# Optimization experiments

Hardware: AMD Instinct MI355X
Metric: run time of the kernel (lower is better)

Reference implementation:

```python
import jax, jax.numpy as jnp
import numpy as np

B, NH, T, D = 2, 16, 2048, 64

def setup_inputs() -> dict:
    key = jax.random.key(0)
    kq, kk, kv = jax.random.split(key, 3)
    Q = jax.random.normal(kq, (B, NH, T, D), dtype=jnp.float32)
    K = jax.random.normal(kk, (B, NH, T, D), dtype=jnp.float32)
    V = jax.random.normal(kv, (B, NH, T, D), dtype=jnp.float32)
    return {"Q": Q, "K": K, "V": V}

def reference(Q, K, V):
    # scores: [B, nh, T, T]
    Dh = Q.shape[-1]
    scale = 1.0 / jnp.sqrt(jnp.asarray(Dh, Q.dtype))
    scores = jnp.einsum('bhtd,bhsd->bhts', Q, K) * scale
    Tq = Q.shape[2]
    causal = jnp.tril(jnp.ones((Tq, Tq), dtype=bool))
    scores = jnp.where(causal, scores, jnp.asarray(-jnp.inf, scores.dtype))
    attn = jax.nn.softmax(scores, axis=-1)
    return jnp.einsum('bhts,bhsd->bhtd', attn, V)
```

## Files before the change

### kernel.cpp

```cpp
#include <hip/hip_runtime.h>
#include <hip/hip_bf16.h>


typedef __bf16 bf16;
typedef __bf16 bf16x2 __attribute__((ext_vector_type(2)));
typedef __bf16 bf16x4 __attribute__((ext_vector_type(4)));
typedef __bf16 bf16x8 __attribute__((ext_vector_type(8)));
typedef float floatx4 __attribute__((ext_vector_type(4)));

#define T_SEQ 2048
#define DH 64
#define TKS 32
#define BHN 32
#define CEXP 0.18033688011112042f

__device__ __forceinline__ void gload16(const bf16* g, bf16* l) {
    __builtin_amdgcn_global_load_lds(
        (const __attribute__((address_space(1))) void*)g,
        (__attribute__((address_space(3))) void*)l, 16, 0, 0);
}

__global__ __launch_bounds__(256) void prep(const float* __restrict__ K,
                                            const float* __restrict__ V,
                                            bf16* __restrict__ Kb,
                                            bf16* __restrict__ Vt) {
    const int bid = (int)blockIdx.x;
    const int tid = (int)threadIdx.x;
    if (bid < 512) {
        size_t i = ((size_t)bid * 256 + tid) * 8;
        #pragma unroll
        for (int it = 0; it < 4; ++it) {
            float4 a = *(const float4*)(K + i + 0);
            float4 b = *(const float4*)(K + i + 4);
            bf16x8 o;
            o[0]=(bf16)(a.x*CEXP); o[1]=(bf16)(a.y*CEXP); o[2]=(bf16)(a.z*CEXP); o[3]=(bf16)(a.w*CEXP);
            o[4]=(bf16)(b.x*CEXP); o[5]=(bf16)(b.y*CEXP); o[6]=(bf16)(b.z*CEXP); o[7]=(bf16)(b.w*CEXP);
            *(bf16x8*)(Kb + i) = o;
            i += (size_t)512 * 256 * 8;
        }
        return;
    }
    __shared__ bf16 tile[2][64][72];
    const int vb = bid - 512;
    const int bh = vb & (BHN - 1);
    const int tp = (vb >> 5) * 128;
    #pragma unroll
    for (int tt = 0; tt < 2; ++tt) {
        const int r = tid >> 2;
        const int c = (tid & 3) * 16;
        const float* s = V + ((size_t)bh * T_SEQ + tp + tt * 64 + r) * DH + c;
        float4 f0 = *(const float4*)(s + 0);
        float4 f1 = *(const float4*)(s + 4);
        float4 f2 = *(const float4*)(s + 8);
        float4 f3 = *(const float4*)(s + 12);
        bf16x8 p0, p1;
        p0[0]=(bf16)f0.x; p0[1]=(bf16)f0.y; p0[2]=(bf16)f0.z; p0[3]=(bf16)f0.w;
        p0[4]=(bf16)f1.x; p0[5]=(bf16)f1.y; p0[6]=(bf16)f1.z; p0[7]=(bf16)f1.w;
        p1[0]=(bf16)f2.x; p1[1]=(bf16)f2.y; p1[2]=(bf16)f2.z; p1[3]=(bf16)f2.w;
        p1[4]=(bf16)f3.x; p1[5]=(bf16)f3.y; p1[6]=(bf16)f3.z; p1[7]=(bf16)f3.w;
        *(bf16x8*)&tile[tt][r][c + 0] = p0;
        *(bf16x8*)&tile[tt][r][c + 8] = p1;
    }
    __syncthreads();
    #pragma unroll
    for (int tt = 0; tt < 2; ++tt) {
        const int d   = tid >> 2;
        const int tch = (tid & 3) * 16;
        bf16x8 o0, o1;
        #pragma unroll
        for (int j = 0; j < 8; ++j) { o0[j] = tile[tt][tch + j][d]; o1[j] = tile[tt][tch + 8 + j][d]; }
        bf16* o = Vt + ((size_t)bh * DH + d) * T_SEQ + tp + tt * 64 + tch;
        *(bf16x8*)(o + 0) = o0;
        *(bf16x8*)(o + 8) = o1;
    }
}

__global__ __launch_bounds__(256, 2)
void fa_fwd(const float* __restrict__ Qg, const bf16* __restrict__ Kb,
            const bf16* __restrict__ Vt, float* __restrict__ Og)
{
    __shared__ __align__(16) bf16 smem[32768];

    const int gid = (int)blockIdx.x;
    const int bh  = gid & (BHN - 1);
    const int m   = gid >> 5;
    const int B   = 64 - 2 * m;
    const int qh  = (31 - m) * 64;
    const int ql  = m * 64;

    const int tid  = (int)threadIdx.x;
    const int wave = tid >> 6;
    const int lane = tid & 63;
    const int quad = lane >> 4;
    const int l16  = lane & 15;
    const int psw  = (l16 >> 1) & 3;

    const int tw0 = (wave < 2) ? wave * 17 : 34 + (wave - 2) * 16;
    const int tw1 = tw0 + ((wave < 2) ? 17 : 16);

    bf16* W = smem + wave * 8192;

    const bf16* Kbh = Kb + (size_t)bh * (T_SEQ * DH);
    const bf16* Vbh = Vt + (size_t)bh * (DH * T_SEQ);
    const size_t qrb = (size_t)bh * T_SEQ;

    const int rl  = lane >> 3;
    const int kch = (lane & 7) ^ (rl & 7);
    const int vr  = lane >> 2;
    const int vch = (lane & 3) ^ ((lane >> 3) & 3);

    bool heavyNow = (tw0 < B);
    int  qbase    = heavyNow ? qh : ql;
    bool hasPark  = false;

    bf16x8 qb[4][2];
    auto loadQ = [&](int qb0) {
        #pragma unroll
        for (int nt = 0; nt < 4; ++nt) {
            const int qrow = qb0 + nt * 16 + l16;
            #pragma unroll
            for (int kk = 0; kk < 2; ++kk) {
                const float* s = Qg + (qrb + qrow) * DH + kk * 32 + quad * 8;
                float4 f0 = *(const float4*)(s);
                float4 f1 = *(const float4*)(s + 4);
                bf16x8 t;
                t[0]=(bf16)f0.x; t[1]=(bf16)f0.y; t[2]=(bf16)f0.z; t[3]=(bf16)f0.w;
                t[4]=(bf16)f1.x; t[5]=(bf16)f1.y; t[6]=(bf16)f1.z; t[7]=(bf16)f1.w;
                qb[nt][kk] = t;
            }
        }
    };
    loadQ(qbase);

    floatx4 oacc[4][4];
    #pragma unroll
    for (int mt = 0; mt < 4; ++mt)
        #pragma unroll
        for (int nt = 0; nt < 4; ++nt) oacc[mt][nt] = (floatx4){0.f,0.f,0.f,0.f};
    float lpart[4] = {0.f, 0.f, 0.f, 0.f};
    bf16x4 parked[16];
    #pragma unroll
    for (int f = 0; f < 16; ++f) parked[f] = (bf16x4){(bf16)0.f,(bf16)0.f,(bf16)0.f,(bf16)0.f};
    float lpark[4] = {0.f, 0.f, 0.f, 0.f};

    auto kTileOf = [&](int t) { return (t < B) ? t : (t - B); };

    auto stageK = [&](int kt, bf16* dst) {
        const bf16* kg = Kbh + (size_t)kt * TKS * DH;
        #pragma unroll
        for (int g = 0; g < 4; ++g)
            gload16(kg + (size_t)(g * 8 + rl) * DH + kch * 8, dst + g * 512);
    };
    auto stageV = [&](int kt, bf16* dst) {
        const bf16* vg = Vbh + kt * TKS;
        #pragma unroll
        for (int g = 0; g < 4; ++g)
            gload16(vg + (size_t)(g * 16 + vr) * T_SEQ + vch * 8, dst + g * 512);
    };

    auto pk2 = [&](float a, float b) -> unsigned {
        bf16x2 h; h[0] = (bf16)a; h[1] = (bf16)b;
        return __builtin_bit_cast(unsigned, h);
    };

    stageK(kTileOf(tw0), W);
    stageV(kTileOf(tw0), W + 4096);

    for (int t = tw0; t < tw1; ++t) {
        if (heavyNow && t == B) {
            #pragma unroll
            for (int f = 0; f < 16; ++f) {
                bf16x4 w;
                #pragma unroll
                for (int e = 0; e < 4; ++e) w[e] = (bf16)oacc[f >> 2][f & 3][e];
                parked[f] = w;
            }
            #pragma unroll
            for (int nt = 0; nt < 4; ++nt) { lpark[nt] = lpart[nt]; lpart[nt] = 0.f; }
            #pragma unroll
            for (int mt = 0; mt < 4; ++mt)
                #pragma unroll
                for (int nt = 0; nt < 4; ++nt) oacc[mt][nt] = (floatx4){0.f,0.f,0.f,0.f};
            hasPark = true;
            heavyNow = false;
            qbase = ql;
            loadQ(ql);
        }

        const int cur = (t - tw0) & 1;
        bf16* Kcur = W + cur * 2048;
        bf16* Vcur = W + 4096 + cur * 2048;
        const int kt = kTileOf(t);
        const int k0 = kt * TKS;

        const bool pf = (t + 1 < tw1);
        if (pf) {
            const int ktn = kTileOf(t + 1);
            stageK(ktn, W + (cur ^ 1) * 2048);
            stageV(ktn, W + 4096 + (cur ^ 1) * 2048);
            __builtin_amdgcn_s_waitcnt(0x0F78);
        } else {
            __builtin_amdgcn_s_waitcnt(0x0F70);
        }

        floatx4 sa[2][4];
        #pragma unroll
        for (int mt = 0; mt < 2; ++mt)
            #pragma unroll
            for (int nt = 0; nt < 4; ++nt) sa[mt][nt] = (floatx4){0.f,0.f,0.f,0.f};
        __builtin_amdgcn_s_setprio(1);
        #pragma unroll
        for (int kk = 0; kk < 2; ++kk) {
            #pragma unroll
            for (int mt = 0; mt < 2; ++mt) {
                bf16x8 kf = *(const bf16x8*)&Kcur[(mt * 16 + l16) * 64 + (((kk * 4 + quad) ^ (l16 & 7)) * 8)];
                #pragma unroll
                for (int nt = 0; nt < 4; ++nt)
                    sa[mt][nt] = __builtin_amdgcn_mfma_f32_16x16x32_bf16(kf, qb[nt][kk], sa[mt][nt], 0, 0, 0);
            }
        }
        __builtin_amdgcn_s_setprio(0);
        bf16x8 vf[4];
        #pragma unroll
        for (int mt = 0; mt < 4; ++mt)
            vf[mt] = *(const bf16x8*)&Vcur[(mt * 16 + l16) * 32 + ((quad ^ psw) * 8)];
        if (k0 + TKS - 1 > qbase) {
            #pragma unroll
            for (int mt = 0; mt < 2; ++mt)
                #pragma unroll
                for (int nt = 0; nt < 4; ++nt) {
                    const int qg = qbase + nt * 16 + l16;
                    #pragma unroll
                    for (int r = 0; r < 4; ++r) {
                        const int keyg = k0 + mt * 16 + quad * 4 + r;
                        if (keyg > qg) sa[mt][nt][r] = -INFINITY;
                    }
                }
        }
        bf16x8 pfr[4];
        #pragma unroll
        for (int nt = 0; nt < 4; ++nt) {
            float p0[4], p1[4];
            #pragma unroll
            for (int r = 0; r < 4; ++r) {
                p0[r] = __builtin_amdgcn_exp2f(sa[0][nt][r]);
                p1[r] = __builtin_amdgcn_exp2f(sa[1][nt][r]);
                lpart[nt] += p0[r] + p1[r];
            }
            unsigned X0 = pk2(p0[0], p0[1]);
            unsigned X1 = pk2(p0[2], p0[3]);
            unsigned Y0 = pk2(p1[0], p1[1]);
            unsigned Y1 = pk2(p1[2], p1[3]);
            asm("v_permlane32_swap_b32 %0, %1" : "+v"(X0), "+v"(Y0));
            asm("v_permlane16_swap_b32 %0, %1" : "+v"(X0), "+v"(Y0));
            asm("v_permlane32_swap_b32 %0, %1" : "+v"(X1), "+v"(Y1));
            asm("v_permlane16_swap_b32 %0, %1" : "+v"(X1), "+v"(Y1));
            uint4 u; u.x = X0; u.y = X1; u.z = Y0; u.w = Y1;
            pfr[nt] = __builtin_bit_cast(bf16x8, u);
        }
        __builtin_amdgcn_s_setprio(1);
        #pragma unroll
        for (int mt = 0; mt < 4; ++mt) {
            #pragma unroll
            for (int nt = 0; nt < 4; ++nt)
                oacc[mt][nt] = __builtin_amdgcn_mfma_f32_16x16x32_bf16(vf[mt], pfr[nt], oacc[mt][nt], 0, 0, 0);
        }
        __builtin_amdgcn_s_setprio(0);
    }

    __syncthreads();
    const bool hH = (tw0 < B);
    const bool hL = (tw1 > B);
    if (wave >= 1 && hH) {
        bf16* a = smem + (wave - 1) * 4608;
        float* al = (float*)(a + 4096);
        #pragma unroll
        for (int f = 0; f < 16; ++f) {
            bf16x4 w;
            if (hasPark) w = parked[f];
            else {
                #pragma unroll
                for (int e = 0; e < 4; ++e) w[e] = (bf16)oacc[f >> 2][f & 3][e];
            }
            *(bf16x4*)&a[(f * 64 + lane) * 4] = w;
        }
        #pragma unroll
        for (int nt = 0; nt < 4; ++nt)
            al[nt * 64 + lane] = hasPark ? lpark[nt] : lpart[nt];
    }
    if (wave >= 2 && hL) {
        bf16* a = smem + (wave + 1) * 4608;
        float* al = (float*)(a + 4096);
        #pragma unroll
        for (int f = 0; f < 16; ++f) {
            bf16x4 w;
            #pragma unroll
            for (int e = 0; e < 4; ++e) w[e] = (bf16)oacc[f >> 2][f & 3][e];
            *(bf16x4*)&a[(f * 64 + lane) * 4] = w;
        }
        #pragma unroll
        for (int nt = 0; nt < 4; ++nt)
            al[nt * 64 + lane] = lpart[nt];
    }
    __syncthreads();

    if (wave <= 1) {
        int qfin;
        if (wave == 0) {
            qfin = qh;
            const int nA = (B > 50) ? 3 : ((B > 34) ? 2 : 1);
            for (int i = 0; i < nA; ++i) {
                const bf16* a = smem + i * 4608;
                const float* al = (const float*)(a + 4096);
                #pragma unroll
                for (int f = 0; f < 16; ++f) {
                    bf16x4 w = *(const bf16x4*)&a[(f * 64 + lane) * 4];
                    #pragma unroll
                    for (int e = 0; e < 4; ++e) oacc[f >> 2][f & 3][e] += (float)w[e];
                }
                #pragma unroll
                for (int nt = 0; nt < 4; ++nt) lpart[nt] += al[nt * 64 + lane];
            }
        } else {
            qfin = ql;
            #pragma unroll
            for (int mt = 0; mt < 4; ++mt)
                #pragma unroll
                for (int nt = 0; nt < 4; ++nt) oacc[mt][nt] = (floatx4){0.f,0.f,0.f,0.f};
            #pragma unroll
            for (int nt = 0; nt < 4; ++nt) lpart[nt] = 0.f;
            const int i0 = (B < 50) ? 3 : 4;
            for (int i = i0; i <= 4; ++i) {
                const bf16* a = smem + i * 4608;
                const float* al = (const float*)(a + 4096);
                #pragma unroll
                for (int f = 0; f < 16; ++f) {
                    bf16x4 w = *(const bf16x4*)&a[(f * 64 + lane) * 4];
                    #pragma unroll
                    for (int e = 0; e < 4; ++e) oacc[f >> 2][f & 3][e] += (float)w[e];
                }
                #pragma unroll
                for (int nt = 0; nt < 4; ++nt) lpart[nt] += al[nt * 64 + lane];
            }
        }
        float invl[4];
        #pragma unroll
        for (int nt = 0; nt < 4; ++nt) {
            float v = lpart[nt];
            v += __shfl_xor(v, 16);
            v += __shfl_xor(v, 32);
            invl[nt] = 1.0f / v;
        }
        #pragma unroll
        for (int nt = 0; nt < 4; ++nt) {
            const size_t qrow = qrb + qfin + nt * 16 + l16;
            #pragma unroll
            for (int mt = 0; mt < 4; ++mt) {
                float4 o;
                o.x = oacc[mt][nt][0] * invl[nt];
                o.y = oacc[mt][nt][1] * invl[nt];
                o.z = oacc[mt][nt][2] * invl[nt];
                o.w = oacc[mt][nt][3] * invl[nt];
                *(float4*)&Og[qrow * DH + mt * 16 + quad * 4] = o;
            }
        }
    }
}

extern "C" void kernel_launch(void* const* d_in, const int* in_sizes, int n_in,
                              void* d_out, int out_size, void* d_ws, size_t ws_size,
                              hipStream_t stream) {
    const float* Q = (const float*)d_in[0];
    const float* K = (const float*)d_in[1];
    const float* V = (const float*)d_in[2];
    float* O = (float*)d_out;
    (void)in_sizes; (void)n_in; (void)out_size; (void)ws_size;

    const size_t nelem = (size_t)BHN * T_SEQ * DH;
    bf16* Kbf = (bf16*)d_ws;
    bf16* Vtb = Kbf + nelem;

    prep<<<dim3(1024), dim3(256), 0, stream>>>(K, V, Kbf, Vtb);
    fa_fwd<<<dim3(512), dim3(256), 0, stream>>>(Q, Kbf, Vtb, O);
}
```

Measured before the change: 120.8 us.

## Software-pipeline QK^T one tile ahead, overlapping with softmax and PV MFMAs

Restructures the flash-attention inner loop so the S=K·Q MFMAs for tile t+1 are issued after the softmax of tile t and before its PV MFMAs. K is now prefetched two tiles ahead and V one tile ahead. The Q reload and accumulator parking at the heavy/light boundary are moved to match the new pipeline depth. The aim is to hide exp/permlane latency behind matrix work. In exchange, the sa registers stay live across iterations, which raises register pressure, and the wait-count and buffer-index logic becomes more involved.

```diff
diff --git a/kernel.cpp b/kernel.cpp
--- a/kernel.cpp
+++ b/kernel.cpp
@@ -163,67 +163,39 @@
         return __builtin_bit_cast(unsigned, h);
     };
 
-    stageK(kTileOf(tw0), W);
-    stageV(kTileOf(tw0), W + 4096);
+    const floatx4 zf4 = {0.f, 0.f, 0.f, 0.f};
+    floatx4 sa[2][4];
+    auto computeS = [&](const bf16* Kbuf) {
+        #pragma unroll
+        for (int kk = 0; kk < 2; ++kk)
+            #pragma unroll
+            for (int mt = 0; mt < 2; ++mt) {
+                bf16x8 kf = *(const bf16x8*)&Kbuf[(mt * 16 + l16) * 64 + (((kk * 4 + quad) ^ (l16 & 7)) * 8)];
+                #pragma unroll
+                for (int nt = 0; nt < 4; ++nt)
+                    sa[mt][nt] = __builtin_amdgcn_mfma_f32_16x16x32_bf16(
+                        kf, qb[nt][kk], (kk == 0) ? zf4 : sa[mt][nt], 0, 0, 0);
+            }
+    };
+
+    stageK(kTileOf(tw0),     W + (tw0 & 1) * 2048);
+    stageV(kTileOf(tw0),     W + 4096 + (tw0 & 1) * 2048);
+    stageK(kTileOf(tw0 + 1), W + ((tw0 + 1) & 1) * 2048);
+    __builtin_amdgcn_s_waitcnt(0x0F78);
+    computeS(W + (tw0 & 1) * 2048);
 
     for (int t = tw0; t < tw1; ++t) {
-        if (heavyNow && t == B) {
-            #pragma unroll
-            for (int f = 0; f < 16; ++f) {
-                bf16x4 w;
-                #pragma unroll
-                for (int e = 0; e < 4; ++e) w[e] = (bf16)oacc[f >> 2][f & 3][e];
-                parked[f] = w;
-            }
-            #pragma unroll
-            for (int nt = 0; nt < 4; ++nt) { lpark[nt] = lpart[nt]; lpart[nt] = 0.f; }
-            #pragma unroll
-            for (int mt = 0; mt < 4; ++mt)
-                #pragma unroll
-                for (int nt = 0; nt < 4; ++nt) oacc[mt][nt] = (floatx4){0.f,0.f,0.f,0.f};
-            hasPark = true;
-            heavyNow = false;
-            qbase = ql;
-            loadQ(ql);
-        }
-
-        const int cur = (t - tw0) & 1;
-        bf16* Kcur = W + cur * 2048;
-        bf16* Vcur = W + 4096 + cur * 2048;
-        const int kt = kTileOf(t);
-        const int k0 = kt * TKS;
-
-        const bool pf = (t + 1 < tw1);
-        if (pf) {
-            const int ktn = kTileOf(t + 1);
-            stageK(ktn, W + (cur ^ 1) * 2048);
-            stageV(ktn, W + 4096 + (cur ^ 1) * 2048);
-            __builtin_amdgcn_s_waitcnt(0x0F78);
-        } else {
-            __builtin_amdgcn_s_waitcnt(0x0F70);
-        }
-
-        floatx4 sa[2][4];
-        #pragma unroll
-        for (int mt = 0; mt < 2; ++mt)
-            #pragma unroll
-            for (int nt = 0; nt < 4; ++nt) sa[mt][nt] = (floatx4){0.f,0.f,0.f,0.f};
-        __builtin_amdgcn_s_setprio(1);
-        #pragma unroll
-        for (int kk = 0; kk < 2; ++kk) {
-            #pragma unroll
-            for (int mt = 0; mt < 2; ++mt) {
-                bf16x8 kf = *(const bf16x8*)&Kcur[(mt * 16 + l16) * 64 + (((kk * 4 + quad) ^ (l16 & 7)) * 8)];
-                #pragma unroll
-                for (int nt = 0; nt < 4; ++nt)
-                    sa[mt][nt] = __builtin_amdgcn_mfma_f32_16x16x32_bf16(kf, qb[nt][kk], sa[mt][nt], 0, 0, 0);
-            }
-        }
-        __builtin_amdgcn_s_setprio(0);
-        bf16x8 vf[4];
-        #pragma unroll
-        for (int mt = 0; mt < 4; ++mt)
-            vf[mt] = *(const bf16x8*)&Vcur[(mt * 16 + l16) * 32 + ((quad ^ psw) * 8)];
+        const bool hasN  = (t + 1 < tw1);
+        const bool hasN2 = (t + 2 < tw1);
+
+        if (hasN2) stageK(kTileOf(t + 2), W + (t & 1) * 2048);
+        if (hasN)  stageV(kTileOf(t + 1), W + 4096 + ((t + 1) & 1) * 2048);
+        if (hasN2)     __builtin_amdgcn_s_waitcnt(0x0F78);
+        else if (hasN) __builtin_amdgcn_s_waitcnt(0x0F74);
+        else           __builtin_amdgcn_s_waitcnt(0x0F70);
+
+        const int k0 = kTileOf(t) * TKS;
+
         if (k0 + TKS - 1 > qbase) {
             #pragma unroll
             for (int mt = 0; mt < 2; ++mt)
@@ -258,6 +230,12 @@
             uint4 u; u.x = X0; u.y = X1; u.z = Y0; u.w = Y1;
             pfr[nt] = __builtin_bit_cast(bf16x8, u);
         }
+        if (hasN) computeS(W + ((t + 1) & 1) * 2048);
+        if (heavyNow && t + 2 == B) loadQ(ql);
+        bf16x8 vf[4];
+        #pragma unroll
+        for (int mt = 0; mt < 4; ++mt)
+            vf[mt] = *(const bf16x8*)&W[4096 + (t & 1) * 2048 + (mt * 16 + l16) * 32 + ((quad ^ psw) * 8)];
         __builtin_amdgcn_s_setprio(1);
         #pragma unroll
         for (int mt = 0; mt < 4; ++mt) {
@@ -266,6 +244,24 @@
                 oacc[mt][nt] = __builtin_amdgcn_mfma_f32_16x16x32_bf16(vf[mt], pfr[nt], oacc[mt][nt], 0, 0, 0);
         }
         __builtin_amdgcn_s_setprio(0);
+        if (heavyNow && t + 1 == B) {
+            #pragma unroll
+            for (int f = 0; f < 16; ++f) {
+                bf16x4 w;
+                #pragma unroll
+                for (int e = 0; e < 4; ++e) w[e] = (bf16)oacc[f >> 2][f & 3][e];
+                parked[f] = w;
+            }
+            #pragma unroll
+            for (int nt = 0; nt < 4; ++nt) { lpark[nt] = lpart[nt]; lpart[nt] = 0.f; }
+            #pragma unroll
+            for (int mt = 0; mt < 4; ++mt)
+                #pragma unroll
+                for (int nt = 0; nt < 4; ++nt) oacc[mt][nt] = (floatx4){0.f,0.f,0.f,0.f};
+            hasPark = true;
+            heavyNow = false;
+            qbase = ql;
+        }
     }
 
     __syncthreads();
```

Result: slower. 125.1 us (+3.6%).
